# Performance work log

Measured on AMD Instinct MI355X. Metric: run time of the kernel, lower is better.

Reference implementation:

```python
import jax, jax.numpy as jnp
import numpy as np

# FlowNetC correlation hyperparameters (match init_kwargs)
PAD = 20          # pad_size
KSIZE = 1         # kernel_size (1x1 patches -> plain per-pixel dot over channels)
MAXD = 20         # max_displacement
STRIDE1 = 1       # output grid stride
STRIDE2 = 2       # displacement stride


def setup_inputs() -> dict:
    key = jax.random.key(0)
    k1, k2 = jax.random.split(key)
    B, C, H, W = 16, 256, 48, 64
    return {
        "input1": jax.random.normal(k1, (B, C, H, W), dtype=jnp.float32),
        "input2": jax.random.normal(k2, (B, C, H, W), dtype=jnp.float32),
    }


def _correlation(in1, in2):
    B, C, H, W = in1.shape
    # pad input2 spatially; max_displacement == pad_size so every shifted
    # window of size (H, W) stays in-bounds of the padded map.
    pad2 = jnp.pad(in2, ((0, 0), (0, 0), (PAD, PAD), (PAD, PAD)))
    disps = np.arange(-MAXD, MAXD + 1, STRIDE2)  # 21 offsets per axis
    offsets = jnp.asarray(
        [(PAD + dy, PAD + dx) for dy in disps for dx in disps], dtype=jnp.int32
    )  # [D=441, 2]

    in1s = in1[:, :, ::STRIDE1, ::STRIDE1]  # output-grid view of input1

    def one_displacement(off):
        # shifted (H, W) window of padded input2 at displacement (dy, dx)
        sl = jax.lax.dynamic_slice(pad2, (0, 0, off[0], off[1]), (B, C, H, W))
        sl = sl[:, :, ::STRIDE1, ::STRIDE1]
        # per-pixel dot product over channels
        return jnp.einsum('bchw,bchw->bhw', in1s, sl)

    # lax.map keeps memory low: one [B,C,H,W] slice live at a time
    out = jax.lax.map(one_displacement, offsets)  # [D, B, Ho, Wo]
    sumelems = KSIZE * KSIZE * C  # CUDA kernel normalizes by patch elem count
    return jnp.transpose(out, (1, 0, 2, 3)) / sumelems  # [B, D, Ho, Wo]


def reference(input1, input2):
    return _correlation(input1, input2)
```

## Files before the change

kernel.cpp:

```cpp
#include <hip/hip_runtime.h>
#include <stdint.h>

#define NB 16
#define NC 256
#define NH 48
#define NW 64
#define ND 21
#define HW (NH * NW)
#define ROW_ELEMS (NW * NC)
#define NXCD 8
#define NWG (NB * NH)
#define SO_LD 65
#define SO_SZ (ND * SO_LD)

typedef __bf16 bf16x8 __attribute__((ext_vector_type(8)));
typedef float f32x4 __attribute__((ext_vector_type(4)));

__device__ __forceinline__ int xcd_wg(int orig) {
    return (orig & (NXCD - 1)) * (NWG / NXCD) + (orig >> 3);
}

__device__ __forceinline__ int sw_addr(int x, int chunk) {
    int cs = (chunk & ~7) | ((chunk ^ x) & 7);
    return x * 256 + (cs << 3);
}
__device__ __forceinline__ int posx(int x) { return ((x & 1) << 5) | (x >> 1); }

__device__ __forceinline__ int frag_off(int w, int kb, int l) {
    return w * 4096 + kb * 512 + ((l ^ ((w & 3) << 1)) << 3);
}

__device__ __forceinline__ bf16x8 load_pack8(const float* __restrict__ p, int cbase) {
    bf16x8 v;
#pragma unroll
    for (int j = 0; j < 8; ++j)
        v[j] = (__bf16)p[(size_t)(cbase + j) * HW];
    return v;
}

__global__ void __launch_bounds__(256, 4)
convert_in2(const float* __restrict__ in2, unsigned short* __restrict__ ws) {
    __shared__ unsigned short s[ROW_ELEMS];
    const int tid = threadIdx.x;
    const int wg = xcd_wg(blockIdx.x);
    const int b = wg / NH, y = wg % NH;
    const int x = tid & 63, g0 = tid >> 6;
    const int par = x & 1, m_lo = (x >> 1) & 15, nt = x >> 5;
    const int w = (nt << 1) | par;
    const float* p = in2 + ((size_t)b * NC * NH + y) * NW + x;
#pragma unroll
    for (int i = 0; i < 8; ++i) {
        const int chunk = g0 * 8 + i;
        const int kb = chunk >> 2, quad = chunk & 3;
        const int l = (quad << 4) | m_lo;
        bf16x8 v = load_pack8(p, chunk * 8);
        *(bf16x8*)&s[frag_off(w, kb, l)] = v;
    }
    __syncthreads();
    unsigned short* wr = ws + ((size_t)b * NH + y) * ROW_ELEMS;
#pragma unroll
    for (int i = 0; i < 8; ++i) {
        const int e = (i * 256 + tid) * 8;
        *(bf16x8*)(wr + e) = *(const bf16x8*)(s + e);
    }
}

__global__ void __launch_bounds__(768, 3)
corr_main(const float* __restrict__ in1, const unsigned short* __restrict__ ws,
          float* __restrict__ out) {
    __shared__ __align__(16) unsigned char smem[65536];
    unsigned short* bbuf  = (unsigned short*)smem;
    float*          soutf = (float*)(smem + 32768);
    unsigned short* areg0 = (unsigned short*)smem;
    unsigned short* areg1 = (unsigned short*)(smem + 32768);

    const int tid  = threadIdx.x;
    const int bid  = blockIdx.x;
    const int xcd  = bid & 7;
    const int u    = bid >> 3;
    const int b    = 2 * xcd + (u >> 4);
    const int v    = u & 15;
    const int P    = v & 1, g = (v >> 1) & 3, half = v >> 3;
    const int y0   = 12 * g + P;
    const int lane = tid & 63, wave = tid >> 6;
    const int m_lo = lane & 15, quad = lane >> 4;
    const int par  = wave & 1, yy = wave >> 1;
    const int y    = y0 + 2 * yy;

    const int lo = max(y0 - 20, P);
    const int hi = min(y0 + 30, 46 + P);
    const int n  = ((hi - lo) >> 1) + 1;
    const int n0 = (n + 1) >> 1;
    const int lo_h = half ? (lo + 2 * n0) : lo;
    const int nh   = half ? (n - n0) : n0;

    const unsigned short* wsb = ws + (size_t)b * NH * ROW_ELEMS;

    bf16x8 Bst[3];
    {
        const unsigned short* row = wsb + (size_t)lo_h * ROW_ELEMS;
        Bst[0] = *(const bf16x8*)&row[tid * 8];
        Bst[1] = *(const bf16x8*)&row[(768 + tid) * 8];
        if (tid < 512) Bst[2] = *(const bf16x8*)&row[(1536 + tid) * 8];
    }

    bf16x8 afrag[2][8];
#pragma unroll 1
    for (int rnd = 0; rnd < 3; ++rnd) {
        const int yA = y0 + 4 * rnd;
#pragma unroll
        for (int i = 0; i < 6; ++i) {
            const int uu = i * 768 + tid;
            if (uu < 4096) {
                const int row = uu >> 11, cu = uu & 2047;
                const int x = cu & 63, chunk = cu >> 6;
                const float* p = in1 + ((size_t)b * NC * NH + (yA + 2 * row)) * NW + x;
                bf16x8 vv = load_pack8(p, chunk * 8);
                unsigned short* dst = row ? areg1 : areg0;
                *(bf16x8*)&dst[sw_addr(posx(x), chunk)] = vv;
            }
        }
        __asm__ __volatile__("s_waitcnt lgkmcnt(0)\n\ts_barrier" ::: "memory");
        if ((yy >> 1) == rnd) {
            const unsigned short* src = (yy & 1) ? areg1 : areg0;
            const int pos0 = par * 32 + m_lo;
#pragma unroll
            for (int kb = 0; kb < 8; ++kb) {
                afrag[0][kb] = *(const bf16x8*)&src[sw_addr(pos0,      4 * kb + quad)];
                afrag[1][kb] = *(const bf16x8*)&src[sw_addr(pos0 + 16, 4 * kb + quad)];
            }
        }
        __asm__ __volatile__("s_waitcnt lgkmcnt(0)\n\ts_barrier" ::: "memory");
    }

    *(bf16x8*)&bbuf[tid * 8] = Bst[0];
    *(bf16x8*)&bbuf[(768 + tid) * 8] = Bst[1];
    if (tid < 512) *(bf16x8*)&bbuf[(1536 + tid) * 8] = Bst[2];
    for (int i = tid; i < 6 * SO_SZ; i += 768) soutf[i] = 0.0f;

    float* outyy = out + (size_t)b * (ND * ND) * HW + (size_t)y * NW;
    const int d0 = (y >= 20) ? 0 : ((21 - y) >> 1);
    const int d1 = min(20, (67 - y) >> 1);
    const int zlo = half ? (d1 + 1) : 0;
    const int zhi = half ? ND : d0;
    const int t2  = par * 64 + lane;
    for (int z = zlo; z < zhi; ++z) {
        float* ob = outyy + (size_t)z * ND * HW;
#pragma unroll
        for (int i = 0; i < 11; ++i) {
            const int e = i * 128 + t2;
            if (e < ND * NW)
                __builtin_nontemporal_store(0.0f, &ob[(size_t)(e >> 6) * HW + (e & 63)]);
        }
    }
    __asm__ __volatile__("s_waitcnt lgkmcnt(0)\n\ts_barrier" ::: "memory");

    const float scale = 1.0f / 256.0f;
    const int boff0 = frag_off((0 << 1) | par, 0, lane);
    const int boff1 = frag_off((1 << 1) | par, 0, lane);

    for (int k = 0; k < nh; ++k) {
        const int ys = lo_h + 2 * k;
        if (k + 1 < nh) {
            const unsigned short* row = wsb + (size_t)(ys + 2) * ROW_ELEMS;
            Bst[0] = *(const bf16x8*)&row[tid * 8];
            Bst[1] = *(const bf16x8*)&row[(768 + tid) * 8];
            if (tid < 512) Bst[2] = *(const bf16x8*)&row[(1536 + tid) * 8];
        }
        const int dyi = ((ys - y) >> 1) + 10;
        const bool valid = (unsigned)dyi <= 20u;

        if (valid) {
            f32x4 a00 = {0,0,0,0}, a01 = {0,0,0,0}, a10 = {0,0,0,0}, a11 = {0,0,0,0};
#pragma unroll
            for (int kb = 0; kb < 8; ++kb) {
                bf16x8 b0 = *(const bf16x8*)&bbuf[boff0 + kb * 512];
                bf16x8 b1 = *(const bf16x8*)&bbuf[boff1 + kb * 512];
                a00 = __builtin_amdgcn_mfma_f32_16x16x32_bf16(afrag[0][kb], b0, a00, 0, 0, 0);
                a10 = __builtin_amdgcn_mfma_f32_16x16x32_bf16(afrag[1][kb], b0, a10, 0, 0, 0);
                a01 = __builtin_amdgcn_mfma_f32_16x16x32_bf16(afrag[0][kb], b1, a01, 0, 0, 0);
                a11 = __builtin_amdgcn_mfma_f32_16x16x32_bf16(afrag[1][kb], b1, a11, 0, 0, 0);
            }
            float* sp = soutf + yy * SO_SZ;
#pragma unroll
            for (int mm = 0; mm < 2; ++mm)
#pragma unroll
            for (int nn = 0; nn < 2; ++nn)
#pragma unroll
            for (int r = 0; r < 4; ++r) {
                const int xh  = 16 * mm + 4 * quad + r;
                const int dxi = (16 * nn + m_lo) - xh + 10;
                const float vv = mm == 0 ? (nn == 0 ? a00[r] : a01[r])
                                         : (nn == 0 ? a10[r] : a11[r]);
                if ((unsigned)dxi <= 20u)
                    sp[dxi * SO_LD + 2 * xh + par] = vv;
            }
        }
        __asm__ __volatile__("s_waitcnt lgkmcnt(0)\n\ts_barrier" ::: "memory");

        if (k + 1 < nh) {
            *(bf16x8*)&bbuf[tid * 8] = Bst[0];
            *(bf16x8*)&bbuf[(768 + tid) * 8] = Bst[1];
            if (tid < 512) *(bf16x8*)&bbuf[(1536 + tid) * 8] = Bst[2];
        }
        if (valid) {
            const float* sp = soutf + yy * SO_SZ;
            float* ob = outyy + (size_t)dyi * ND * HW;
#pragma unroll
            for (int i = 0; i < 11; ++i) {
                const int e = i * 128 + t2;
                if (e < ND * NW)
                    __builtin_nontemporal_store(sp[(e >> 6) * SO_LD + (e & 63)] * scale,
                                                &ob[(size_t)(e >> 6) * HW + (e & 63)]);
            }
        }
        __asm__ __volatile__("s_waitcnt lgkmcnt(0)\n\ts_barrier" ::: "memory");
    }
}

__global__ void __launch_bounds__(256, 2)
corr_fallback(const float* __restrict__ in1, const float* __restrict__ in2,
              float* __restrict__ out) {
    __shared__ unsigned short s1[ROW_ELEMS];
    __shared__ unsigned short s2[ROW_ELEMS];
    const int tid = threadIdx.x;
    const int b = blockIdx.x / NH, y = blockIdx.x % NH;
    const int lane = tid & 63, wave = tid >> 6;
    const int m_lo = lane & 15, quad = lane >> 4;
    const int asub = wave >> 1, bsub = wave & 1;
    {
        const int x = tid & 63, g0 = tid >> 6;
        const float* p = in1 + ((size_t)b * NC * NH + y) * NW + x;
        for (int i = 0; i < 8; ++i) {
            const int chunk = g0 * 8 + i;
            bf16x8 v = load_pack8(p, chunk * 8);
            *(bf16x8*)&s1[sw_addr(x, chunk)] = v;
        }
    }
    __syncthreads();
    bf16x8 afrag[2][8];
    for (int mm = 0; mm < 2; ++mm) {
        const int x = 32 * asub + 16 * mm + m_lo;
        for (int kb = 0; kb < 8; ++kb)
            afrag[mm][kb] = *(const bf16x8*)&s1[sw_addr(x, 4 * kb + quad)];
    }
    const float scale = 1.0f / 256.0f;
    for (int dyi = 0; dyi < ND; ++dyi) {
        const int ys = y + 2 * dyi - 20;
        float* ob = out + (((size_t)b * (ND * ND) + (size_t)dyi * ND) * NH + y) * NW;
        if ((unsigned)ys >= (unsigned)NH) {
            for (int i = tid; i < ND * NW; i += 256)
                ob[(size_t)(i >> 6) * HW + (i & 63)] = 0.0f;
            continue;
        }
        __syncthreads();
        {
            const int x = tid & 63, g0 = tid >> 6;
            const float* p = in2 + ((size_t)b * NC * NH + ys) * NW + x;
            for (int i = 0; i < 8; ++i) {
                const int chunk = g0 * 8 + i;
                bf16x8 v = load_pack8(p, chunk * 8);
                *(bf16x8*)&s2[sw_addr(x, chunk)] = v;
            }
        }
        __syncthreads();
        f32x4 acc[2][2];
        for (int mm = 0; mm < 2; ++mm)
            for (int nn = 0; nn < 2; ++nn) acc[mm][nn] = (f32x4){0.f, 0.f, 0.f, 0.f};
        for (int nn = 0; nn < 2; ++nn) {
            const int xpp = 32 * bsub + 16 * nn + m_lo;
            for (int kb = 0; kb < 8; ++kb) {
                bf16x8 bfrag = *(const bf16x8*)&s2[sw_addr(xpp, 4 * kb + quad)];
                acc[0][nn] = __builtin_amdgcn_mfma_f32_16x16x32_bf16(afrag[0][kb], bfrag, acc[0][nn], 0, 0, 0);
                acc[1][nn] = __builtin_amdgcn_mfma_f32_16x16x32_bf16(afrag[1][kb], bfrag, acc[1][nn], 0, 0, 0);
            }
        }
        for (int mm = 0; mm < 2; ++mm)
            for (int nn = 0; nn < 2; ++nn) {
                const int xb = 32 * asub + 16 * mm + 4 * quad;
                const int xpp = 32 * bsub + 16 * nn + m_lo;
                for (int r = 0; r < 4; ++r) {
                    const int x = xb + r, d = xpp - x;
                    if (d >= -20 && d <= 20 && !(d & 1))
                        ob[(size_t)((d + 20) >> 1) * HW + x] = acc[mm][nn][r] * scale;
                }
            }
        for (int i = tid; i < ND * 20; i += 256) {
            const int dxi = i / 20, j = i - dxi * 20;
            const int dx = 2 * dxi - 20, a = dx < 0 ? -dx : dx;
            if (j < a) {
                const int x = dx < 0 ? j : (NW - dx + j);
                ob[(size_t)dxi * HW + x] = 0.0f;
            }
        }
    }
}

extern "C" void kernel_launch(void* const* d_in, const int* in_sizes, int n_in,
                              void* d_out, int out_size, void* d_ws, size_t ws_size,
                              hipStream_t stream) {
    const float* in1 = (const float*)d_in[0];
    const float* in2 = (const float*)d_in[1];
    float* out = (float*)d_out;
    const size_t need = (size_t)NB * NH * ROW_ELEMS * sizeof(unsigned short);
    if (ws_size >= need) {
        convert_in2<<<dim3(NWG), dim3(256), 0, stream>>>(in2, (unsigned short*)d_ws);
        corr_main<<<dim3(256), dim3(768), 0, stream>>>(in1, (const unsigned short*)d_ws, out);
    } else {
        corr_fallback<<<dim3(NWG), dim3(256), 0, stream>>>(in1, in2, out);
    }
}
```

Baseline: 49.38 us.

## Give each wave two output rows and regroup blocks into 16-row bands

Each block now covers 8 output rows with 512 threads. Every wave holds A fragments for two rows (ya, yb) and reuses each B tile from LDS across both rows. Blocks are split into 16-row groups with 3- or 2-way splits of the input2 row range, replacing the old 12-row groups with halves. The aim is to raise MFMA work per B-tile LDS load and per streamed input2 row. The cost is more registers for afrag, larger shared memory (about 76KB), and fewer resident waves per CU.

```diff
diff --git a/kernel.cpp b/kernel.cpp
--- a/kernel.cpp
+++ b/kernel.cpp
@@ -65,92 +65,99 @@
     }
 }
 
-__global__ void __launch_bounds__(768, 3)
+__global__ void __launch_bounds__(512, 2)
 corr_main(const float* __restrict__ in1, const unsigned short* __restrict__ ws,
           float* __restrict__ out) {
-    __shared__ __align__(16) unsigned char smem[65536];
+    __shared__ __align__(16) unsigned char smem[76448];
     unsigned short* bbuf  = (unsigned short*)smem;
     float*          soutf = (float*)(smem + 32768);
-    unsigned short* areg0 = (unsigned short*)smem;
-    unsigned short* areg1 = (unsigned short*)(smem + 32768);
-
-    const int tid  = threadIdx.x;
-    const int bid  = blockIdx.x;
-    const int xcd  = bid & 7;
-    const int u    = bid >> 3;
-    const int b    = 2 * xcd + (u >> 4);
-    const int v    = u & 15;
-    const int P    = v & 1, g = (v >> 1) & 3, half = v >> 3;
-    const int y0   = 12 * g + P;
+    unsigned short* reg0  = (unsigned short*)smem;
+    unsigned short* reg1  = (unsigned short*)(smem + 32768);
+
+    const int tid = threadIdx.x;
+    const int bid = blockIdx.x;
+    const int xcd = bid & 7;
+    const int t   = bid >> 3;
+    const int b   = 2 * xcd + (t & 1);
+    const int u   = t >> 1;
+    const int P   = u & 1;
+    const int s   = u >> 1;
+    const int g   = s < 3 ? 0 : (s < 6 ? 1 : 2);
+    const int sub = s - (g == 0 ? 0 : (g == 1 ? 3 : 6));
+    const int nsplit = (g == 2) ? 2 : 3;
+    const int y0  = 16 * g + P;
+
     const int lane = tid & 63, wave = tid >> 6;
     const int m_lo = lane & 15, quad = lane >> 4;
-    const int par  = wave & 1, yy = wave >> 1;
-    const int y    = y0 + 2 * yy;
+    const int par  = wave & 1, yp = wave >> 1;
+    const int ya   = y0 + 4 * yp, yb = ya + 2;
 
     const int lo = max(y0 - 20, P);
-    const int hi = min(y0 + 30, 46 + P);
+    const int hi = min(y0 + 34, 46 + P);
     const int n  = ((hi - lo) >> 1) + 1;
-    const int n0 = (n + 1) >> 1;
-    const int lo_h = half ? (lo + 2 * n0) : lo;
-    const int nh   = half ? (n - n0) : n0;
+    const int chunk = (n + nsplit - 1) / nsplit;
+    const int lo_h  = lo + 2 * chunk * sub;
+    const int nh    = min(chunk, n - chunk * sub);
 
     const unsigned short* wsb = ws + (size_t)b * NH * ROW_ELEMS;
 
-    bf16x8 Bst[3];
+    bf16x8 Bst[4];
     {
         const unsigned short* row = wsb + (size_t)lo_h * ROW_ELEMS;
-        Bst[0] = *(const bf16x8*)&row[tid * 8];
-        Bst[1] = *(const bf16x8*)&row[(768 + tid) * 8];
-        if (tid < 512) Bst[2] = *(const bf16x8*)&row[(1536 + tid) * 8];
-    }
-
-    bf16x8 afrag[2][8];
-#pragma unroll 1
-    for (int rnd = 0; rnd < 3; ++rnd) {
-        const int yA = y0 + 4 * rnd;
-#pragma unroll
-        for (int i = 0; i < 6; ++i) {
-            const int uu = i * 768 + tid;
-            if (uu < 4096) {
-                const int row = uu >> 11, cu = uu & 2047;
-                const int x = cu & 63, chunk = cu >> 6;
-                const float* p = in1 + ((size_t)b * NC * NH + (yA + 2 * row)) * NW + x;
-                bf16x8 vv = load_pack8(p, chunk * 8);
-                unsigned short* dst = row ? areg1 : areg0;
-                *(bf16x8*)&dst[sw_addr(posx(x), chunk)] = vv;
-            }
+#pragma unroll
+        for (int k2 = 0; k2 < 4; ++k2)
+            Bst[k2] = *(const bf16x8*)&row[(tid + 512 * k2) * 8];
+    }
+
+    bf16x8 afrag[2][2][8];
+#pragma unroll
+    for (int rnd = 0; rnd < 4; ++rnd) {
+        const int rya = y0 + 4 * rnd;
+#pragma unroll
+        for (int i = 0; i < 4; ++i) {
+            const int pack = i * 512 + tid;
+            const int x = pack & 63, ch = pack >> 6;
+            const float* pa = in1 + ((size_t)b * NC * NH + rya) * NW + x;
+            const float* pb = in1 + ((size_t)b * NC * NH + rya + 2) * NW + x;
+            bf16x8 va = load_pack8(pa, ch * 8);
+            bf16x8 vb = load_pack8(pb, ch * 8);
+            *(bf16x8*)&reg0[sw_addr(posx(x), ch)] = va;
+            *(bf16x8*)&reg1[sw_addr(posx(x), ch)] = vb;
         }
         __asm__ __volatile__("s_waitcnt lgkmcnt(0)\n\ts_barrier" ::: "memory");
-        if ((yy >> 1) == rnd) {
-            const unsigned short* src = (yy & 1) ? areg1 : areg0;
-            const int pos0 = par * 32 + m_lo;
-#pragma unroll
-            for (int kb = 0; kb < 8; ++kb) {
-                afrag[0][kb] = *(const bf16x8*)&src[sw_addr(pos0,      4 * kb + quad)];
-                afrag[1][kb] = *(const bf16x8*)&src[sw_addr(pos0 + 16, 4 * kb + quad)];
+        if (yp == rnd) {
+#pragma unroll
+            for (int mm = 0; mm < 2; ++mm) {
+                const int pos = par * 32 + 16 * mm + m_lo;
+#pragma unroll
+                for (int kb = 0; kb < 8; ++kb) {
+                    afrag[0][mm][kb] = *(const bf16x8*)&reg0[sw_addr(pos, 4 * kb + quad)];
+                    afrag[1][mm][kb] = *(const bf16x8*)&reg1[sw_addr(pos, 4 * kb + quad)];
+                }
             }
         }
         __asm__ __volatile__("s_waitcnt lgkmcnt(0)\n\ts_barrier" ::: "memory");
     }
 
-    *(bf16x8*)&bbuf[tid * 8] = Bst[0];
-    *(bf16x8*)&bbuf[(768 + tid) * 8] = Bst[1];
-    if (tid < 512) *(bf16x8*)&bbuf[(1536 + tid) * 8] = Bst[2];
-    for (int i = tid; i < 6 * SO_SZ; i += 768) soutf[i] = 0.0f;
-
-    float* outyy = out + (size_t)b * (ND * ND) * HW + (size_t)y * NW;
-    const int d0 = (y >= 20) ? 0 : ((21 - y) >> 1);
-    const int d1 = min(20, (67 - y) >> 1);
-    const int zlo = half ? (d1 + 1) : 0;
-    const int zhi = half ? ND : d0;
-    const int t2  = par * 64 + lane;
-    for (int z = zlo; z < zhi; ++z) {
-        float* ob = outyy + (size_t)z * ND * HW;
-#pragma unroll
-        for (int i = 0; i < 11; ++i) {
-            const int e = i * 128 + t2;
-            if (e < ND * NW)
-                __builtin_nontemporal_store(0.0f, &ob[(size_t)(e >> 6) * HW + (e & 63)]);
+#pragma unroll
+    for (int k2 = 0; k2 < 4; ++k2)
+        *(bf16x8*)&bbuf[(tid + 512 * k2) * 8] = Bst[k2];
+    for (int i = tid; i < 8 * SO_SZ; i += 512) soutf[i] = 0.0f;
+
+    float* outb = out + (size_t)b * (ND * ND) * HW;
+    const int yd   = par ? yb : ya;
+    const int pidx = 2 * yp + par;
+    float* oyd = outb + (size_t)yd * NW;
+
+    if (sub == 0) {
+        const int d0 = (yd >= 20) ? 0 : ((21 - yd) >> 1);
+        const int d1 = min(20, (67 - yd) >> 1);
+        for (int z = 0; z < ND; ++z) {
+            if (z >= d0 && z <= d1) continue;
+            float* ob = oyd + (size_t)z * ND * HW;
+#pragma unroll
+            for (int i2 = 0; i2 < ND; ++i2)
+                __builtin_nontemporal_store(0.0f, &ob[(size_t)i2 * HW + lane]);
         }
     }
     __asm__ __volatile__("s_waitcnt lgkmcnt(0)\n\ts_barrier" ::: "memory");
@@ -163,56 +170,82 @@
         const int ys = lo_h + 2 * k;
         if (k + 1 < nh) {
             const unsigned short* row = wsb + (size_t)(ys + 2) * ROW_ELEMS;
-            Bst[0] = *(const bf16x8*)&row[tid * 8];
-            Bst[1] = *(const bf16x8*)&row[(768 + tid) * 8];
-            if (tid < 512) Bst[2] = *(const bf16x8*)&row[(1536 + tid) * 8];
-        }
-        const int dyi = ((ys - y) >> 1) + 10;
-        const bool valid = (unsigned)dyi <= 20u;
-
-        if (valid) {
-            f32x4 a00 = {0,0,0,0}, a01 = {0,0,0,0}, a10 = {0,0,0,0}, a11 = {0,0,0,0};
+#pragma unroll
+            for (int k2 = 0; k2 < 4; ++k2)
+                Bst[k2] = *(const bf16x8*)&row[(tid + 512 * k2) * 8];
+        }
+        const int dyia = ((ys - ya) >> 1) + 10;
+        const int dyib = dyia - 1;
+        const bool va = (unsigned)dyia <= 20u;
+        const bool vb = (unsigned)dyib <= 20u;
+
+        f32x4 c000 = {0,0,0,0}, c001 = {0,0,0,0}, c010 = {0,0,0,0}, c011 = {0,0,0,0};
+        f32x4 c100 = {0,0,0,0}, c101 = {0,0,0,0}, c110 = {0,0,0,0}, c111 = {0,0,0,0};
+        if (va || vb) {
 #pragma unroll
             for (int kb = 0; kb < 8; ++kb) {
                 bf16x8 b0 = *(const bf16x8*)&bbuf[boff0 + kb * 512];
                 bf16x8 b1 = *(const bf16x8*)&bbuf[boff1 + kb * 512];
-                a00 = __builtin_amdgcn_mfma_f32_16x16x32_bf16(afrag[0][kb], b0, a00, 0, 0, 0);
-                a10 = __builtin_amdgcn_mfma_f32_16x16x32_bf16(afrag[1][kb], b0, a10, 0, 0, 0);
-                a01 = __builtin_amdgcn_mfma_f32_16x16x32_bf16(afrag[0][kb], b1, a01, 0, 0, 0);
-                a11 = __builtin_amdgcn_mfma_f32_16x16x32_bf16(afrag[1][kb], b1, a11, 0, 0, 0);
-            }
-            float* sp = soutf + yy * SO_SZ;
+                if (va) {
+                    c000 = __builtin_amdgcn_mfma_f32_16x16x32_bf16(afrag[0][0][kb], b0, c000, 0, 0, 0);
+                    c001 = __builtin_amdgcn_mfma_f32_16x16x32_bf16(afrag[0][0][kb], b1, c001, 0, 0, 0);
+                    c010 = __builtin_amdgcn_mfma_f32_16x16x32_bf16(afrag[0][1][kb], b0, c010, 0, 0, 0);
+                    c011 = __builtin_amdgcn_mfma_f32_16x16x32_bf16(afrag[0][1][kb], b1, c011, 0, 0, 0);
+                }
+                if (vb) {
+                    c100 = __builtin_amdgcn_mfma_f32_16x16x32_bf16(afrag[1][0][kb], b0, c100, 0, 0, 0);
+                    c101 = __builtin_amdgcn_mfma_f32_16x16x32_bf16(afrag[1][0][kb], b1, c101, 0, 0, 0);
+                    c110 = __builtin_amdgcn_mfma_f32_16x16x32_bf16(afrag[1][1][kb], b0, c110, 0, 0, 0);
+                    c111 = __builtin_amdgcn_mfma_f32_16x16x32_bf16(afrag[1][1][kb], b1, c111, 0, 0, 0);
+                }
+            }
+        }
+
+        if (va) {
+            float* sp = soutf + (2 * yp) * SO_SZ;
 #pragma unroll
             for (int mm = 0; mm < 2; ++mm)
 #pragma unroll
             for (int nn = 0; nn < 2; ++nn)
 #pragma unroll
             for (int r = 0; r < 4; ++r) {
-                const int xh  = 16 * mm + 4 * quad + r;
-                const int dxi = (16 * nn + m_lo) - xh + 10;
-                const float vv = mm == 0 ? (nn == 0 ? a00[r] : a01[r])
-                                         : (nn == 0 ? a10[r] : a11[r]);
-                if ((unsigned)dxi <= 20u)
-                    sp[dxi * SO_LD + 2 * xh + par] = vv;
+                const int xh = 16 * mm + 4 * quad + r;
+                const int dxi = 16 * nn + m_lo - xh + 10;
+                const float vv = mm == 0 ? (nn == 0 ? c000[r] : c001[r])
+                                         : (nn == 0 ? c010[r] : c011[r]);
+                if ((unsigned)dxi <= 20u) sp[dxi * SO_LD + 2 * xh + par] = vv;
+            }
+        }
+        if (vb) {
+            float* sp = soutf + (2 * yp + 1) * SO_SZ;
+#pragma unroll
+            for (int mm = 0; mm < 2; ++mm)
+#pragma unroll
+            for (int nn = 0; nn < 2; ++nn)
+#pragma unroll
+            for (int r = 0; r < 4; ++r) {
+                const int xh = 16 * mm + 4 * quad + r;
+                const int dxi = 16 * nn + m_lo - xh + 10;
+                const float vv = mm == 0 ? (nn == 0 ? c100[r] : c101[r])
+                                         : (nn == 0 ? c110[r] : c111[r]);
+                if ((unsigned)dxi <= 20u) sp[dxi * SO_LD + 2 * xh + par] = vv;
             }
         }
         __asm__ __volatile__("s_waitcnt lgkmcnt(0)\n\ts_barrier" ::: "memory");
 
         if (k + 1 < nh) {
-            *(bf16x8*)&bbuf[tid * 8] = Bst[0];
-            *(bf16x8*)&bbuf[(768 + tid) * 8] = Bst[1];
-            if (tid < 512) *(bf16x8*)&bbuf[(1536 + tid) * 8] = Bst[2];
-        }
-        if (valid) {
-            const float* sp = soutf + yy * SO_SZ;
-            float* ob = outyy + (size_t)dyi * ND * HW;
-#pragma unroll
-            for (int i = 0; i < 11; ++i) {
-                const int e = i * 128 + t2;
-                if (e < ND * NW)
-                    __builtin_nontemporal_store(sp[(e >> 6) * SO_LD + (e & 63)] * scale,
-                                                &ob[(size_t)(e >> 6) * HW + (e & 63)]);
-            }
+#pragma unroll
+            for (int k2 = 0; k2 < 4; ++k2)
+                *(bf16x8*)&bbuf[(tid + 512 * k2) * 8] = Bst[k2];
+        }
+        const int dyid = par ? dyib : dyia;
+        if ((unsigned)dyid <= 20u) {
+            const float* sp = soutf + pidx * SO_SZ;
+            float* ob = oyd + (size_t)dyid * ND * HW;
+#pragma unroll
+            for (int i2 = 0; i2 < ND; ++i2)
+                __builtin_nontemporal_store(sp[i2 * SO_LD + lane] * scale,
+                                            &ob[(size_t)i2 * HW + lane]);
         }
         __asm__ __volatile__("s_waitcnt lgkmcnt(0)\n\ts_barrier" ::: "memory");
     }
@@ -305,7 +338,7 @@
     const size_t need = (size_t)NB * NH * ROW_ELEMS * sizeof(unsigned short);
     if (ws_size >= need) {
         convert_in2<<<dim3(NWG), dim3(256), 0, stream>>>(in2, (unsigned short*)d_ws);
-        corr_main<<<dim3(256), dim3(768), 0, stream>>>(in1, (const unsigned short*)d_ws, out);
+        corr_main<<<dim3(256), dim3(512), 0, stream>>>(in1, (const unsigned short*)d_ws, out);
     } else {
         corr_fallback<<<dim3(NWG), dim3(256), 0, stream>>>(in1, in2, out);
     }
```

After: 55.01 us. +11.4%, slower.

## Double-buffer B rows and output staging via direct global-to-LDS loads

Applied to the files above, without the earlier changes.

Replaces the register-staged B-row prefetch with global_load_lds DMA into a double-buffered 64KB LDS region, issued by 8 loader waves. The output staging buffer is also double-buffered, so each iteration drains the previous row's results while computing the current one, cutting the per-iteration barriers from two to one. LDS use grows to 128KB per block and launch bounds drop to one block per CU, trading occupancy for overlap. The vmcnt-based waits must correctly cover both the LDS DMA and the outstanding nontemporal stores.

```diff
diff --git a/kernel.cpp b/kernel.cpp
--- a/kernel.cpp
+++ b/kernel.cpp
@@ -16,6 +16,10 @@
 typedef __bf16 bf16x8 __attribute__((ext_vector_type(8)));
 typedef float f32x4 __attribute__((ext_vector_type(4)));
 
+#define GLOAD_LDS16(g, l) __builtin_amdgcn_global_load_lds(               \
+    (const __attribute__((address_space(1))) unsigned int*)(g),           \
+    (__attribute__((address_space(3))) unsigned int*)(l), 16, 0, 0)
+
 __device__ __forceinline__ int xcd_wg(int orig) {
     return (orig & (NXCD - 1)) * (NWG / NXCD) + (orig >> 3);
 }
@@ -65,23 +69,23 @@
     }
 }
 
-__global__ void __launch_bounds__(768, 3)
+__global__ void __launch_bounds__(768, 1)
 corr_main(const float* __restrict__ in1, const unsigned short* __restrict__ ws,
           float* __restrict__ out) {
-    __shared__ __align__(16) unsigned char smem[65536];
+    __shared__ __align__(16) unsigned char smem[131072];
     unsigned short* bbuf  = (unsigned short*)smem;
-    float*          soutf = (float*)(smem + 32768);
-    unsigned short* areg0 = (unsigned short*)smem;
-    unsigned short* areg1 = (unsigned short*)(smem + 32768);
-
-    const int tid  = threadIdx.x;
-    const int bid  = blockIdx.x;
-    const int xcd  = bid & 7;
-    const int u    = bid >> 3;
-    const int b    = 2 * xcd + (u >> 4);
-    const int v    = u & 15;
-    const int P    = v & 1, g = (v >> 1) & 3, half = v >> 3;
-    const int y0   = 12 * g + P;
+    float*          soutf = (float*)(smem + 65536);
+    unsigned short* reg0  = (unsigned short*)(smem + 65536);
+    unsigned short* reg1  = (unsigned short*)(smem + 98304);
+
+    const int tid = threadIdx.x;
+    const int bid = blockIdx.x;
+    const int xcd = bid & 7;
+    const int u   = bid >> 3;
+    const int b   = 2 * xcd + (u >> 4);
+    const int v   = u & 15;
+    const int P   = v & 1, g = (v >> 1) & 3, half = v >> 3;
+    const int y0  = 12 * g + P;
     const int lane = tid & 63, wave = tid >> 6;
     const int m_lo = lane & 15, quad = lane >> 4;
     const int par  = wave & 1, yy = wave >> 1;
@@ -95,13 +99,17 @@
     const int nh   = half ? (n - n0) : n0;
 
     const unsigned short* wsb = ws + (size_t)b * NH * ROW_ELEMS;
-
-    bf16x8 Bst[3];
-    {
+    const bool loader = (wave < 8);
+
+    if (loader) {
         const unsigned short* row = wsb + (size_t)lo_h * ROW_ELEMS;
-        Bst[0] = *(const bf16x8*)&row[tid * 8];
-        Bst[1] = *(const bf16x8*)&row[(768 + tid) * 8];
-        if (tid < 512) Bst[2] = *(const bf16x8*)&row[(1536 + tid) * 8];
+        asm volatile("" ::: "memory");
+#pragma unroll
+        for (int i = 0; i < 4; ++i) {
+            const int ch = wave * 4 + i;
+            GLOAD_LDS16(row + ch * 512 + lane * 8, bbuf + ch * 512);
+        }
+        asm volatile("" ::: "memory");
     }
 
     bf16x8 afrag[2][8];
@@ -116,13 +124,13 @@
                 const int x = cu & 63, chunk = cu >> 6;
                 const float* p = in1 + ((size_t)b * NC * NH + (yA + 2 * row)) * NW + x;
                 bf16x8 vv = load_pack8(p, chunk * 8);
-                unsigned short* dst = row ? areg1 : areg0;
+                unsigned short* dst = row ? reg1 : reg0;
                 *(bf16x8*)&dst[sw_addr(posx(x), chunk)] = vv;
             }
         }
         __asm__ __volatile__("s_waitcnt lgkmcnt(0)\n\ts_barrier" ::: "memory");
         if ((yy >> 1) == rnd) {
-            const unsigned short* src = (yy & 1) ? areg1 : areg0;
+            const unsigned short* src = (yy & 1) ? reg1 : reg0;
             const int pos0 = par * 32 + m_lo;
 #pragma unroll
             for (int kb = 0; kb < 8; ++kb) {
@@ -133,10 +141,7 @@
         __asm__ __volatile__("s_waitcnt lgkmcnt(0)\n\ts_barrier" ::: "memory");
     }
 
-    *(bf16x8*)&bbuf[tid * 8] = Bst[0];
-    *(bf16x8*)&bbuf[(768 + tid) * 8] = Bst[1];
-    if (tid < 512) *(bf16x8*)&bbuf[(1536 + tid) * 8] = Bst[2];
-    for (int i = tid; i < 6 * SO_SZ; i += 768) soutf[i] = 0.0f;
+    for (int i = tid; i < 12 * SO_SZ; i += 768) soutf[i] = 0.0f;
 
     float* outyy = out + (size_t)b * (ND * ND) * HW + (size_t)y * NW;
     const int d0 = (y >= 20) ? 0 : ((21 - y) >> 1);
@@ -153,6 +158,7 @@
                 __builtin_nontemporal_store(0.0f, &ob[(size_t)(e >> 6) * HW + (e & 63)]);
         }
     }
+    if (loader) asm volatile("s_waitcnt vmcnt(0)" ::: "memory");
     __asm__ __volatile__("s_waitcnt lgkmcnt(0)\n\ts_barrier" ::: "memory");
 
     const float scale = 1.0f / 256.0f;
@@ -161,12 +167,21 @@
 
     for (int k = 0; k < nh; ++k) {
         const int ys = lo_h + 2 * k;
-        if (k + 1 < nh) {
+        const int cur = k & 1;
+        const unsigned short* bb = bbuf + cur * 16384;
+
+        if (k + 1 < nh && loader) {
             const unsigned short* row = wsb + (size_t)(ys + 2) * ROW_ELEMS;
-            Bst[0] = *(const bf16x8*)&row[tid * 8];
-            Bst[1] = *(const bf16x8*)&row[(768 + tid) * 8];
-            if (tid < 512) Bst[2] = *(const bf16x8*)&row[(1536 + tid) * 8];
-        }
+            unsigned short* dstb = bbuf + (cur ^ 1) * 16384;
+            asm volatile("" ::: "memory");
+#pragma unroll
+            for (int i = 0; i < 4; ++i) {
+                const int ch = wave * 4 + i;
+                GLOAD_LDS16(row + ch * 512 + lane * 8, dstb + ch * 512);
+            }
+            asm volatile("" ::: "memory");
+        }
+
         const int dyi = ((ys - y) >> 1) + 10;
         const bool valid = (unsigned)dyi <= 20u;
 
@@ -174,14 +189,14 @@
             f32x4 a00 = {0,0,0,0}, a01 = {0,0,0,0}, a10 = {0,0,0,0}, a11 = {0,0,0,0};
 #pragma unroll
             for (int kb = 0; kb < 8; ++kb) {
-                bf16x8 b0 = *(const bf16x8*)&bbuf[boff0 + kb * 512];
-                bf16x8 b1 = *(const bf16x8*)&bbuf[boff1 + kb * 512];
+                bf16x8 b0 = *(const bf16x8*)&bb[boff0 + kb * 512];
+                bf16x8 b1 = *(const bf16x8*)&bb[boff1 + kb * 512];
                 a00 = __builtin_amdgcn_mfma_f32_16x16x32_bf16(afrag[0][kb], b0, a00, 0, 0, 0);
                 a10 = __builtin_amdgcn_mfma_f32_16x16x32_bf16(afrag[1][kb], b0, a10, 0, 0, 0);
                 a01 = __builtin_amdgcn_mfma_f32_16x16x32_bf16(afrag[0][kb], b1, a01, 0, 0, 0);
                 a11 = __builtin_amdgcn_mfma_f32_16x16x32_bf16(afrag[1][kb], b1, a11, 0, 0, 0);
             }
-            float* sp = soutf + yy * SO_SZ;
+            float* sp = soutf + (cur * 6 + yy) * SO_SZ;
 #pragma unroll
             for (int mm = 0; mm < 2; ++mm)
 #pragma unroll
@@ -196,16 +211,12 @@
                     sp[dxi * SO_LD + 2 * xh + par] = vv;
             }
         }
-        __asm__ __volatile__("s_waitcnt lgkmcnt(0)\n\ts_barrier" ::: "memory");
-
-        if (k + 1 < nh) {
-            *(bf16x8*)&bbuf[tid * 8] = Bst[0];
-            *(bf16x8*)&bbuf[(768 + tid) * 8] = Bst[1];
-            if (tid < 512) *(bf16x8*)&bbuf[(1536 + tid) * 8] = Bst[2];
-        }
-        if (valid) {
-            const float* sp = soutf + yy * SO_SZ;
-            float* ob = outyy + (size_t)dyi * ND * HW;
+
+        const int dyp = dyi - 1;
+        const bool drain = (k > 0) && ((unsigned)dyp <= 20u);
+        if (drain) {
+            const float* sp = soutf + ((cur ^ 1) * 6 + yy) * SO_SZ;
+            float* ob = outyy + (size_t)dyp * ND * HW;
 #pragma unroll
             for (int i = 0; i < 11; ++i) {
                 const int e = i * 128 + t2;
@@ -214,7 +225,26 @@
                                                 &ob[(size_t)(e >> 6) * HW + (e & 63)]);
             }
         }
-        __asm__ __volatile__("s_waitcnt lgkmcnt(0)\n\ts_barrier" ::: "memory");
+        if (drain)
+            asm volatile("s_waitcnt lgkmcnt(0) vmcnt(11)\n\ts_barrier" ::: "memory");
+        else
+            asm volatile("s_waitcnt lgkmcnt(0) vmcnt(0)\n\ts_barrier" ::: "memory");
+    }
+
+    {
+        const int ysL = lo_h + 2 * (nh - 1);
+        const int dyL = ((ysL - y) >> 1) + 10;
+        if ((unsigned)dyL <= 20u) {
+            const float* sp = soutf + (((nh - 1) & 1) * 6 + yy) * SO_SZ;
+            float* ob = outyy + (size_t)dyL * ND * HW;
+#pragma unroll
+            for (int i = 0; i < 11; ++i) {
+                const int e = i * 128 + t2;
+                if (e < ND * NW)
+                    __builtin_nontemporal_store(sp[(e >> 6) * SO_LD + (e & 63)] * scale,
+                                                &ob[(size_t)(e >> 6) * HW + (e & 63)]);
+            }
+        }
     }
 }
 
```

After: 48.25 us (median of 2 runs). 2.3% less time.

## Repartition correlation work into 576 smaller blocks covering 4 rows and a third of the source rows

Applied to the files above, without the earlier changes.

The main correlation kernel moves from 256 workgroups of 768 threads (6 output rows, source rows split in two halves) to 576 workgroups of 512 threads (4 output rows, source rows split in thirds). The A-fragment staging now reuses the B buffer region and LDS use shrinks to about 54 KB, so more workgroups can be resident per CU. The intent is better load balance and occupancy across CUs. The cost is more redundant in1 fragment loading and more workgroups each doing their own setup.

```diff
diff --git a/kernel.cpp b/kernel.cpp
--- a/kernel.cpp
+++ b/kernel.cpp
@@ -65,92 +65,88 @@
     }
 }
 
-__global__ void __launch_bounds__(768, 3)
+__global__ void __launch_bounds__(512, 4)
 corr_main(const float* __restrict__ in1, const unsigned short* __restrict__ ws,
           float* __restrict__ out) {
-    __shared__ __align__(16) unsigned char smem[65536];
+    __shared__ __align__(16) unsigned char smem[54608];
     unsigned short* bbuf  = (unsigned short*)smem;
     float*          soutf = (float*)(smem + 32768);
-    unsigned short* areg0 = (unsigned short*)smem;
-    unsigned short* areg1 = (unsigned short*)(smem + 32768);
-
-    const int tid  = threadIdx.x;
-    const int bid  = blockIdx.x;
-    const int xcd  = bid & 7;
-    const int u    = bid >> 3;
-    const int b    = 2 * xcd + (u >> 4);
-    const int v    = u & 15;
-    const int P    = v & 1, g = (v >> 1) & 3, half = v >> 3;
-    const int y0   = 12 * g + P;
+
+    const int tid = threadIdx.x;
+    const int bid = blockIdx.x;
+    const int xcd = bid & 7;
+    const int r   = bid >> 3;
+    const int b   = 2 * xcd + (r >= 36 ? 1 : 0);
+    const int v   = r - (r >= 36 ? 36 : 0);
+    const int P   = v & 1;
+    const int w2  = v >> 1;
+    const int g   = w2 % 6, ti = w2 / 6;
+    const int y0  = 8 * g + P;
+
     const int lane = tid & 63, wave = tid >> 6;
     const int m_lo = lane & 15, quad = lane >> 4;
     const int par  = wave & 1, yy = wave >> 1;
     const int y    = y0 + 2 * yy;
 
     const int lo = max(y0 - 20, P);
-    const int hi = min(y0 + 30, 46 + P);
+    const int hi = min(y0 + 26, 46 + P);
     const int n  = ((hi - lo) >> 1) + 1;
-    const int n0 = (n + 1) >> 1;
-    const int lo_h = half ? (lo + 2 * n0) : lo;
-    const int nh   = half ? (n - n0) : n0;
+    const int q  = (n + 2) / 3;
+    const int lo_t = lo + 2 * q * ti;
+    const int nh   = min(q, n - q * ti);
 
     const unsigned short* wsb = ws + (size_t)b * NH * ROW_ELEMS;
 
-    bf16x8 Bst[3];
+    bf16x8 Bst[4];
     {
-        const unsigned short* row = wsb + (size_t)lo_h * ROW_ELEMS;
-        Bst[0] = *(const bf16x8*)&row[tid * 8];
-        Bst[1] = *(const bf16x8*)&row[(768 + tid) * 8];
-        if (tid < 512) Bst[2] = *(const bf16x8*)&row[(1536 + tid) * 8];
+        const unsigned short* row = wsb + (size_t)lo_t * ROW_ELEMS;
+#pragma unroll
+        for (int k2 = 0; k2 < 4; ++k2)
+            Bst[k2] = *(const bf16x8*)&row[(tid + 512 * k2) * 8];
     }
 
     bf16x8 afrag[2][8];
 #pragma unroll 1
-    for (int rnd = 0; rnd < 3; ++rnd) {
-        const int yA = y0 + 4 * rnd;
-#pragma unroll
-        for (int i = 0; i < 6; ++i) {
-            const int uu = i * 768 + tid;
-            if (uu < 4096) {
-                const int row = uu >> 11, cu = uu & 2047;
-                const int x = cu & 63, chunk = cu >> 6;
-                const float* p = in1 + ((size_t)b * NC * NH + (yA + 2 * row)) * NW + x;
-                bf16x8 vv = load_pack8(p, chunk * 8);
-                unsigned short* dst = row ? areg1 : areg0;
-                *(bf16x8*)&dst[sw_addr(posx(x), chunk)] = vv;
-            }
+    for (int rnd = 0; rnd < 4; ++rnd) {
+        const float* pr = in1 + ((size_t)b * NC * NH + (y0 + 2 * rnd)) * NW;
+#pragma unroll
+        for (int i = 0; i < 4; ++i) {
+            const int pk = i * 512 + tid;
+            const int x = pk & 63, ch = pk >> 6;
+            bf16x8 vv = load_pack8(pr + x, ch * 8);
+            *(bf16x8*)&bbuf[sw_addr(posx(x), ch)] = vv;
         }
         __asm__ __volatile__("s_waitcnt lgkmcnt(0)\n\ts_barrier" ::: "memory");
-        if ((yy >> 1) == rnd) {
-            const unsigned short* src = (yy & 1) ? areg1 : areg0;
+        if (yy == rnd) {
             const int pos0 = par * 32 + m_lo;
 #pragma unroll
             for (int kb = 0; kb < 8; ++kb) {
-                afrag[0][kb] = *(const bf16x8*)&src[sw_addr(pos0,      4 * kb + quad)];
-                afrag[1][kb] = *(const bf16x8*)&src[sw_addr(pos0 + 16, 4 * kb + quad)];
+                afrag[0][kb] = *(const bf16x8*)&bbuf[sw_addr(pos0,      4 * kb + quad)];
+                afrag[1][kb] = *(const bf16x8*)&bbuf[sw_addr(pos0 + 16, 4 * kb + quad)];
             }
         }
         __asm__ __volatile__("s_waitcnt lgkmcnt(0)\n\ts_barrier" ::: "memory");
     }
 
-    *(bf16x8*)&bbuf[tid * 8] = Bst[0];
-    *(bf16x8*)&bbuf[(768 + tid) * 8] = Bst[1];
-    if (tid < 512) *(bf16x8*)&bbuf[(1536 + tid) * 8] = Bst[2];
-    for (int i = tid; i < 6 * SO_SZ; i += 768) soutf[i] = 0.0f;
+#pragma unroll
+    for (int k2 = 0; k2 < 4; ++k2)
+        *(bf16x8*)&bbuf[(tid + 512 * k2) * 8] = Bst[k2];
+    for (int i = tid; i < 4 * SO_SZ; i += 512) soutf[i] = 0.0f;
 
     float* outyy = out + (size_t)b * (ND * ND) * HW + (size_t)y * NW;
     const int d0 = (y >= 20) ? 0 : ((21 - y) >> 1);
     const int d1 = min(20, (67 - y) >> 1);
-    const int zlo = half ? (d1 + 1) : 0;
-    const int zhi = half ? ND : d0;
-    const int t2  = par * 64 + lane;
-    for (int z = zlo; z < zhi; ++z) {
-        float* ob = outyy + (size_t)z * ND * HW;
-#pragma unroll
-        for (int i = 0; i < 11; ++i) {
-            const int e = i * 128 + t2;
-            if (e < ND * NW)
-                __builtin_nontemporal_store(0.0f, &ob[(size_t)(e >> 6) * HW + (e & 63)]);
+    const int t2 = par * 64 + lane;
+    if (ti == 0) {
+        for (int z = 0; z < ND; ++z) {
+            if (z >= d0 && z <= d1) continue;
+            float* ob = outyy + (size_t)z * ND * HW;
+#pragma unroll
+            for (int i = 0; i < 11; ++i) {
+                const int e = i * 128 + t2;
+                if (e < ND * NW)
+                    __builtin_nontemporal_store(0.0f, &ob[(size_t)(e >> 6) * HW + (e & 63)]);
+            }
         }
     }
     __asm__ __volatile__("s_waitcnt lgkmcnt(0)\n\ts_barrier" ::: "memory");
@@ -158,17 +154,19 @@
     const float scale = 1.0f / 256.0f;
     const int boff0 = frag_off((0 << 1) | par, 0, lane);
     const int boff1 = frag_off((1 << 1) | par, 0, lane);
+    const int D0 = ((lo_t - y) >> 1) + 10;
 
     for (int k = 0; k < nh; ++k) {
-        const int ys = lo_h + 2 * k;
-        if (k + 1 < nh) {
-            const unsigned short* row = wsb + (size_t)(ys + 2) * ROW_ELEMS;
-            Bst[0] = *(const bf16x8*)&row[tid * 8];
-            Bst[1] = *(const bf16x8*)&row[(768 + tid) * 8];
-            if (tid < 512) Bst[2] = *(const bf16x8*)&row[(1536 + tid) * 8];
-        }
-        const int dyi = ((ys - y) >> 1) + 10;
+        const int dyi = D0 + k;
         const bool valid = (unsigned)dyi <= 20u;
+        const bool more = (k + 1 < nh);
+
+        if (more) {
+            const unsigned short* row = wsb + (size_t)(lo_t + 2 * (k + 1)) * ROW_ELEMS;
+#pragma unroll
+            for (int k2 = 0; k2 < 4; ++k2)
+                Bst[k2] = *(const bf16x8*)&row[(tid + 512 * k2) * 8];
+        }
 
         if (valid) {
             f32x4 a00 = {0,0,0,0}, a01 = {0,0,0,0}, a10 = {0,0,0,0}, a11 = {0,0,0,0};
@@ -187,21 +185,21 @@
 #pragma unroll
             for (int nn = 0; nn < 2; ++nn)
 #pragma unroll
-            for (int r = 0; r < 4; ++r) {
-                const int xh  = 16 * mm + 4 * quad + r;
+            for (int r2 = 0; r2 < 4; ++r2) {
+                const int xh  = 16 * mm + 4 * quad + r2;
                 const int dxi = (16 * nn + m_lo) - xh + 10;
-                const float vv = mm == 0 ? (nn == 0 ? a00[r] : a01[r])
-                                         : (nn == 0 ? a10[r] : a11[r]);
+                const float vv = mm == 0 ? (nn == 0 ? a00[r2] : a01[r2])
+                                         : (nn == 0 ? a10[r2] : a11[r2]);
                 if ((unsigned)dxi <= 20u)
                     sp[dxi * SO_LD + 2 * xh + par] = vv;
             }
         }
         __asm__ __volatile__("s_waitcnt lgkmcnt(0)\n\ts_barrier" ::: "memory");
 
-        if (k + 1 < nh) {
-            *(bf16x8*)&bbuf[tid * 8] = Bst[0];
-            *(bf16x8*)&bbuf[(768 + tid) * 8] = Bst[1];
-            if (tid < 512) *(bf16x8*)&bbuf[(1536 + tid) * 8] = Bst[2];
+        if (more) {
+#pragma unroll
+            for (int k2 = 0; k2 < 4; ++k2)
+                *(bf16x8*)&bbuf[(tid + 512 * k2) * 8] = Bst[k2];
         }
         if (valid) {
             const float* sp = soutf + yy * SO_SZ;
@@ -305,7 +303,7 @@
     const size_t need = (size_t)NB * NH * ROW_ELEMS * sizeof(unsigned short);
     if (ws_size >= need) {
         convert_in2<<<dim3(NWG), dim3(256), 0, stream>>>(in2, (unsigned short*)d_ws);
-        corr_main<<<dim3(256), dim3(768), 0, stream>>>(in1, (const unsigned short*)d_ws, out);
+        corr_main<<<dim3(576), dim3(512), 0, stream>>>(in1, (const unsigned short*)d_ws, out);
     } else {
         corr_fallback<<<dim3(NWG), dim3(256), 0, stream>>>(in1, in2, out);
     }
```

New measurement: 117.0 us. 137% more time.
